# Performance work log

Hardware: AMD Instinct MI355X
Metric: run time of the kernel (lower is better)

Reference implementation:

```python
import jax, jax.numpy as jnp
import numpy as np

N_NODES = 100000
N_EDGES = 1600000
IN_DIM, HID_DIM, OUT_DIM = 128, 128, 64


def setup_inputs() -> dict:
    key = jax.random.key(0)
    k1, k2, k3, k4 = jax.random.split(key, 4)
    x = jax.random.normal(k1, (N_NODES, IN_DIM), dtype=jnp.float32)
    edge_index = jax.random.randint(k2, (2, N_EDGES), 0, N_NODES, dtype=jnp.int32)
    # Glorot-ish init for weights
    W1 = jax.random.normal(k3, (IN_DIM, HID_DIM), dtype=jnp.float32) / np.sqrt(IN_DIM)
    W2 = jax.random.normal(k4, (HID_DIM, OUT_DIM), dtype=jnp.float32) / np.sqrt(HID_DIM)
    b1 = jnp.zeros((HID_DIM,), dtype=jnp.float32)
    b2 = jnp.zeros((OUT_DIM,), dtype=jnp.float32)
    return {"x": x, "edge_index": edge_index, "W1": W1, "b1": b1, "W2": W2, "b2": b2}


def _gcn_norm(edge_index, num_nodes):
    # PyG gcn_norm: add self-loops, symmetric normalization deg^-1/2 A deg^-1/2
    loops = jnp.arange(num_nodes, dtype=edge_index.dtype)
    src = jnp.concatenate([edge_index[0], loops])  # [E+N]
    tgt = jnp.concatenate([edge_index[1], loops])
    deg = jax.ops.segment_sum(jnp.ones_like(tgt, dtype=jnp.float32), tgt,
                              num_segments=num_nodes)
    dinv = jnp.where(deg > 0, jax.lax.rsqrt(deg), 0.0)
    norm = dinv[src] * dinv[tgt]  # [E+N]
    return src, tgt, norm


def _gcn_conv(x, W, b, src, tgt, norm, num_nodes):
    h = x @ W                              # [N, D_out] transform first (GCNConv order)
    msg = norm[:, None] * h[src]           # gather + scale per edge
    agg = jax.ops.segment_sum(msg, tgt, num_segments=num_nodes)  # scatter-add
    return agg + b


def reference(x, edge_index, W1, b1, W2, b2):
    n = x.shape[0]
    src, tgt, norm = _gcn_norm(edge_index, n)
    h = jax.nn.relu(_gcn_conv(x, W1, b1, src, tgt, norm, n))
    out = _gcn_conv(h, W2, b2, src, tgt, norm, n)
    return out
```

## Files before the change

### kernel.cpp

```cpp
#include <hip/hip_runtime.h>


typedef unsigned int uint;
typedef unsigned short ushort;
typedef __attribute__((ext_vector_type(8))) short bf16x8;
typedef __attribute__((ext_vector_type(8))) ushort u16x8;
typedef __attribute__((ext_vector_type(4))) float f32x4;

#define BSHIFT 8
#define MAXBK  512
#define NB     256
#define CAP    8192

__device__ inline ushort f2bf(float f) {
    uint u = __float_as_uint(f);
    return (ushort)((u + 0x7fffu + ((u >> 16) & 1u)) >> 16);
}
__device__ inline float bf_lo(uint u) { return __uint_as_float(u << 16); }
__device__ inline float bf_hi(uint u) { return __uint_as_float(u & 0xffff0000u); }

__global__ __launch_bounds__(256) void hist_kernel(const int* __restrict__ tgt,
                                                   int* __restrict__ counts,
                                                   int E, int chunk, int nbk) {
    __shared__ int hist[MAXBK];
    int t = threadIdx.x, b = blockIdx.x;
    for (int i = t; i < nbk; i += 256) hist[i] = 0;
    __syncthreads();
    int s = b * chunk, e = min(E, s + chunk);
    int i = s + t * 4;
    for (; i + 3 < e; i += 1024) {
        int4 tv = *(const int4*)&tgt[i];
        atomicAdd(&hist[tv.x >> BSHIFT], 1);
        atomicAdd(&hist[tv.y >> BSHIFT], 1);
        atomicAdd(&hist[tv.z >> BSHIFT], 1);
        atomicAdd(&hist[tv.w >> BSHIFT], 1);
    }
    if (i < e)
        for (int k = i; k < e; ++k) atomicAdd(&hist[tgt[k] >> BSHIFT], 1);
    __syncthreads();
    for (int i2 = t; i2 < nbk; i2 += 256) counts[i2 * NB + b] = hist[i2];
}

__global__ __launch_bounds__(256) void scan_partial(const int* __restrict__ in,
                                                    int* __restrict__ bsum, int M) {
    int t = threadIdx.x, b = blockIdx.x;
    int base = b * 1024 + t * 4;
    int s = 0;
#pragma unroll
    for (int k = 0; k < 4; ++k) s += (base + k < M) ? in[base + k] : 0;
#pragma unroll
    for (int off = 32; off > 0; off >>= 1) s += __shfl_down(s, off, 64);
    __shared__ int ws[4];
    if ((t & 63) == 0) ws[t >> 6] = s;
    __syncthreads();
    if (t == 0) bsum[b] = ws[0] + ws[1] + ws[2] + ws[3];
}

__global__ __launch_bounds__(256) void scan_final_counts(int* __restrict__ counts,
                                                         const int* __restrict__ bsum,
                                                         int M) {
    int t = threadIdx.x, b = blockIdx.x;
    int lane = t & 63, wid = t >> 6;
    int p = 0;
    for (int i = t; i < b; i += 256) p += bsum[i];
#pragma unroll
    for (int off = 32; off > 0; off >>= 1) p += __shfl_down(p, off, 64);
    __shared__ int ps[4];
    if (lane == 0) ps[wid] = p;
    __syncthreads();
    int pre = ps[0] + ps[1] + ps[2] + ps[3];

    int base = b * 1024 + t * 4;
    int d[4];
#pragma unroll
    for (int k = 0; k < 4; ++k) d[k] = (base + k < M) ? counts[base + k] : 0;
    int tot = d[0] + d[1] + d[2] + d[3];
    int incl = tot;
#pragma unroll
    for (int off = 1; off < 64; off <<= 1) {
        int u = __shfl_up(incl, off, 64);
        if (lane >= off) incl += u;
    }
    __shared__ int wsum[4];
    if (lane == 63) wsum[wid] = incl;
    __syncthreads();
    int woff = 0;
    for (int w = 0; w < wid; ++w) woff += wsum[w];
    int run = incl - tot + woff + pre;
#pragma unroll
    for (int k = 0; k < 4; ++k) {
        if (base + k < M) counts[base + k] = run;
        run += d[k];
    }
}

__global__ __launch_bounds__(256) void bucket_scatter(const int* __restrict__ src,
                                                      const int* __restrict__ tgt,
                                                      const int* __restrict__ offsets,
                                                      int* __restrict__ tmpP,
                                                      int E, int chunk, int nbk) {
    __shared__ int cur[MAXBK];
    int t = threadIdx.x, b = blockIdx.x;
    for (int i = t; i < nbk; i += 256) cur[i] = offsets[i * NB + b];
    __syncthreads();
    int s = b * chunk, e = min(E, s + chunk);
    int i = s + t * 4;
    for (; i + 3 < e; i += 1024) {
        int4 sv = *(const int4*)&src[i];
        int4 tv = *(const int4*)&tgt[i];
        int p0 = atomicAdd(&cur[tv.x >> BSHIFT], 1);
        tmpP[p0] = (sv.x << BSHIFT) | (tv.x & 255);
        int p1 = atomicAdd(&cur[tv.y >> BSHIFT], 1);
        tmpP[p1] = (sv.y << BSHIFT) | (tv.y & 255);
        int p2 = atomicAdd(&cur[tv.z >> BSHIFT], 1);
        tmpP[p2] = (sv.z << BSHIFT) | (tv.z & 255);
        int p3 = atomicAdd(&cur[tv.w >> BSHIFT], 1);
        tmpP[p3] = (sv.w << BSHIFT) | (tv.w & 255);
    }
    if (i < e) {
        for (int k = i; k < e; ++k) {
            int tg = tgt[k];
            int p = atomicAdd(&cur[tg >> BSHIFT], 1);
            tmpP[p] = (src[k] << BSHIFT) | (tg & 255);
        }
    }
}

__global__ __launch_bounds__(256) void bucket_finish(const int* __restrict__ tmpP,
                                                     const int* __restrict__ offsets,
                                                     int* __restrict__ rowptr,
                                                     float* __restrict__ dinv,
                                                     int* __restrict__ csr_src,
                                                     int N, int E, int nbk) {
    __shared__ int stage[CAP];
    __shared__ int cnt[256];
    __shared__ int wsum[4];
    int t = threadIdx.x, b = blockIdx.x;
    cnt[t] = 0;
    __syncthreads();
    int s = offsets[b * NB];
    int e = (b + 1 < nbk) ? offsets[(b + 1) * NB] : E;
    int m = e - s;
    for (int i = t; i < m; i += 256) {
        int ed = tmpP[s + i];
        if (i < CAP) stage[i] = ed;
        atomicAdd(&cnt[ed & 255], 1);
    }
    __syncthreads();
    int lane = t & 63, wid = t >> 6;
    int d = cnt[t];
    int incl = d;
#pragma unroll
    for (int off = 1; off < 64; off <<= 1) {
        int u = __shfl_up(incl, off, 64);
        if (lane >= off) incl += u;
    }
    if (lane == 63) wsum[wid] = incl;
    __syncthreads();
    int woff = 0;
    for (int w = 0; w < wid; ++w) woff += wsum[w];
    int excl = s + incl - d + woff;
    int node = b * 256 + t;
    if (node < N) {
        rowptr[node] = excl;
        dinv[node] = rsqrtf((float)d + 1.0f);
    }
    if (b == nbk - 1 && t == 255) rowptr[N] = E;
    cnt[t] = excl;
    __syncthreads();
    for (int i = t; i < m; i += 256) {
        int ed = (i < CAP) ? stage[i] : tmpP[s + i];
        int p = atomicAdd(&cnt[ed & 255], 1);
        csr_src[p] = ed >> BSHIFT;
    }
}

template <int M, typename AT>
__global__ __launch_bounds__(256) void gemm_mfma(const AT* __restrict__ A,
                                                 const float* __restrict__ W,
                                                 const float* __restrict__ dinv,
                                                 ushort* __restrict__ C, int N) {
    constexpr int WTS = 136;
    __shared__ ushort WT[M * WTS];
    const int tid = threadIdx.x;
    for (int i = tid; i < 128 * (M / 4); i += 256) {
        int k = i / (M / 4);
        int n0 = (i % (M / 4)) * 4;
        float4 w = *(const float4*)&W[k * M + n0];
        WT[(n0 + 0) * WTS + k] = f2bf(w.x);
        WT[(n0 + 1) * WTS + k] = f2bf(w.y);
        WT[(n0 + 2) * WTS + k] = f2bf(w.z);
        WT[(n0 + 3) * WTS + k] = f2bf(w.w);
    }
    __syncthreads();

    const int wv = tid >> 6, lane = tid & 63;
    const int quad = lane >> 4, mrow = lane & 15;
    int arow_i = blockIdx.x * 64 + wv * 16 + mrow;
    if (arow_i >= N) arow_i = N - 1;

    f32x4 acc[M / 16];
#pragma unroll
    for (int t = 0; t < M / 16; ++t) acc[t] = (f32x4){0.f, 0.f, 0.f, 0.f};

#pragma unroll
    for (int ks = 0; ks < 4; ++ks) {
        const int k0 = ks * 32 + quad * 8;
        bf16x8 af;
        if constexpr (sizeof(AT) == 4) {
            const float* arow = (const float*)A + (size_t)arow_i * 128;
            float4 a0 = *(const float4*)&arow[k0];
            float4 a1 = *(const float4*)&arow[k0 + 4];
            af[0] = (short)f2bf(a0.x); af[1] = (short)f2bf(a0.y);
            af[2] = (short)f2bf(a0.z); af[3] = (short)f2bf(a0.w);
            af[4] = (short)f2bf(a1.x); af[5] = (short)f2bf(a1.y);
            af[6] = (short)f2bf(a1.z); af[7] = (short)f2bf(a1.w);
        } else {
            af = *(const bf16x8*)((const ushort*)A +
                                  ((size_t)(k0 >> 4) * N + arow_i) * 16 + (k0 & 15));
        }
#pragma unroll
        for (int t = 0; t < M / 16; ++t) {
            int n = t * 16 + mrow;
            bf16x8 bfr = *(const bf16x8*)&WT[n * WTS + k0];
            acc[t] = __builtin_amdgcn_mfma_f32_16x16x32_bf16(af, bfr, acc[t], 0, 0, 0);
        }
    }

    const int orow0 = blockIdx.x * 64 + wv * 16 + quad * 4;
#pragma unroll
    for (int r = 0; r < 4; ++r) {
        int orow = orow0 + r;
        if (orow < N) {
            float dv = dinv[orow];
#pragma unroll
            for (int t = 0; t < M / 16; ++t)
                C[((size_t)t * N + orow) * 16 + mrow] = f2bf(dv * acc[t][r]);
        }
    }
}

template <int D, bool RELU, bool OUTBF>
__global__ __launch_bounds__(128) void gather_sliced(
    const ushort* __restrict__ h, const int* __restrict__ rowptr,
    const int* __restrict__ csr_src, const float* __restrict__ dinv,
    const float* __restrict__ bias, void* __restrict__ outv, int N) {
    constexpr int NS = D / 16;
    constexpr int CAPE = 2048;
    __shared__ int eL[CAPE];
    const int tid = threadIdx.x;
    const int base = blockIdx.x * 64;
    const int bbeg = rowptr[base];
    const int bend = rowptr[min(base + 64, N)];
    const int m = bend - bbeg;
    for (int i = tid; i < m && i < CAPE; i += 128) eL[i] = csr_src[bbeg + i];
    __syncthreads();

    const int node = base + (tid >> 1);
    const int q = tid & 1;
    const int qoff = q * 8;
    const bool alive = node < N;
    int beg = 0, end = 0;
    float di = 0.f;
    if (alive) {
        beg = rowptr[node];
        end = rowptr[node + 1];
        di = dinv[node];
    }

    auto acc8 = [](float* a, uint4 v) {
        a[0] += bf_lo(v.x); a[1] += bf_hi(v.x);
        a[2] += bf_lo(v.y); a[3] += bf_hi(v.y);
        a[4] += bf_lo(v.z); a[5] += bf_hi(v.z);
        a[6] += bf_lo(v.w); a[7] += bf_hi(v.w);
    };

    auto run = [&](auto LD) {
#pragma unroll 1
        for (int s = 0; s < NS; ++s) {
            const ushort* hs = h + (size_t)s * N * 16;
            float acc[8] = {};
            if (alive) {
                int j = beg;
                for (; j + 1 < end; j += 2) {
                    int s0 = LD(j), s1 = LD(j + 1);
                    uint4 va = *(const uint4*)&hs[(size_t)s0 * 16 + qoff];
                    uint4 vb = *(const uint4*)&hs[(size_t)s1 * 16 + qoff];
                    acc8(acc, va);
                    acc8(acc, vb);
                }
                if (j < end) {
                    int s0 = LD(j);
                    acc8(acc, *(const uint4*)&hs[(size_t)s0 * 16 + qoff]);
                }
                acc8(acc, *(const uint4*)&hs[(size_t)node * 16 + qoff]);

                float4 b0 = *(const float4*)&bias[s * 16 + qoff];
                float4 b1 = *(const float4*)&bias[s * 16 + qoff + 4];
                float r[8] = {di * acc[0] + b0.x, di * acc[1] + b0.y,
                              di * acc[2] + b0.z, di * acc[3] + b0.w,
                              di * acc[4] + b1.x, di * acc[5] + b1.y,
                              di * acc[6] + b1.z, di * acc[7] + b1.w};
                if (RELU) {
#pragma unroll
                    for (int k = 0; k < 8; ++k) r[k] = fmaxf(r[k], 0.0f);
                }
                if constexpr (OUTBF) {
                    ushort* out = (ushort*)outv;
                    u16x8 o;
#pragma unroll
                    for (int k = 0; k < 8; ++k) o[k] = f2bf(r[k]);
                    *(u16x8*)&out[((size_t)s * N + node) * 16 + qoff] = o;
                } else {
                    float* out = (float*)outv;
                    *(float4*)&out[(size_t)node * D + s * 16 + qoff] =
                        make_float4(r[0], r[1], r[2], r[3]);
                    *(float4*)&out[(size_t)node * D + s * 16 + qoff + 4] =
                        make_float4(r[4], r[5], r[6], r[7]);
                }
            }
        }
    };

    if (m <= CAPE)
        run([&](int j) { return eL[j - bbeg]; });
    else
        run([&](int j) { return csr_src[j]; });
}

extern "C" void kernel_launch(void* const* d_in, const int* in_sizes, int n_in,
                              void* d_out, int out_size, void* d_ws, size_t ws_size,
                              hipStream_t stream) {
    const float* x  = (const float*)d_in[0];
    const int*   ei = (const int*)d_in[1];
    const float* W1 = (const float*)d_in[2];
    const float* b1 = (const float*)d_in[3];
    const float* W2 = (const float*)d_in[4];
    const float* b2 = (const float*)d_in[5];
    float* out = (float*)d_out;

    const int N = in_sizes[0] / 128;
    const int E = in_sizes[1] / 2;
    const int* src = ei;
    const int* tgt = ei + E;

    const int nbk   = (N + 255) >> BSHIFT;
    const int chunk = (((E + NB - 1) / NB) + 3) & ~3;
    const int Mc    = nbk * NB;

    float* ws = (float*)d_ws;
    const size_t Np = (size_t)((N + 3) & ~3);
    float*  dinv    = ws;
    int*    rowptr  = (int*)(ws + Np);
    int*    counts  = rowptr + Np + 4;
    int*    bsum    = counts + MAXBK * NB;
    int*    csr_src = bsum + 128;
    int*    tmpP    = csr_src + E;
    ushort* h       = (ushort*)(tmpP + E);
    ushort* h1      = h + (size_t)N * 128;
    ushort* h2      = h;

    const int nbc = (Mc + 1023) / 1024;

    hist_kernel<<<NB, 256, 0, stream>>>(tgt, counts, E, chunk, nbk);
    scan_partial<<<nbc, 256, 0, stream>>>(counts, bsum, Mc);
    scan_final_counts<<<nbc, 256, 0, stream>>>(counts, bsum, Mc);
    bucket_scatter<<<NB, 256, 0, stream>>>(src, tgt, counts, tmpP, E, chunk, nbk);
    bucket_finish<<<nbk, 256, 0, stream>>>(tmpP, counts, rowptr, dinv, csr_src, N, E, nbk);

    const int ngb = (N + 63) / 64;

    gemm_mfma<128, float><<<(N + 63) / 64, 256, 0, stream>>>(x, W1, dinv, h, N);
    gather_sliced<128, true, true><<<ngb, 128, 0, stream>>>(
        h, rowptr, csr_src, dinv, b1, h1, N);

    gemm_mfma<64, ushort><<<(N + 63) / 64, 256, 0, stream>>>(h1, W2, dinv, h2, N);
    gather_sliced<64, false, false><<<ngb, 128, 0, stream>>>(
        h2, rowptr, csr_src, dinv, b2, out, N);
}
```

Measured before the change: 343.3 us.

## Split gather feature slices across blocks and widen node tiles

The aggregation kernel now assigns each feature slice to its own block instead of looping over slices inside one block. Each block covers 128 nodes with 256 threads, a larger edge-index staging buffer and a 4-way unrolled neighbour loop. This gives many more concurrent waves to hide the latency of the irregular gathers. In exchange every block reloads the same edge list, and the 64-wide second layer launches 8 slice blocks although it has only 4 slices, so half of those blocks repeat work and write identical results.

```diff
diff --git a/kernel.cpp b/kernel.cpp
--- a/kernel.cpp
+++ b/kernel.cpp
@@ -241,91 +241,85 @@
 }
 
 template <int D, bool RELU, bool OUTBF>
-__global__ __launch_bounds__(128) void gather_sliced(
+__global__ __launch_bounds__(256) void gather_part(
     const ushort* __restrict__ h, const int* __restrict__ rowptr,
     const int* __restrict__ csr_src, const float* __restrict__ dinv,
     const float* __restrict__ bias, void* __restrict__ outv, int N) {
     constexpr int NS = D / 16;
-    constexpr int CAPE = 2048;
+    constexpr int CAPE = 4096;
     __shared__ int eL[CAPE];
     const int tid = threadIdx.x;
-    const int base = blockIdx.x * 64;
+    const int sl = blockIdx.x & 7;
+    const int s  = sl & (NS - 1);
+    const int nb = blockIdx.x >> 3;
+    const int base = nb * 128;
     const int bbeg = rowptr[base];
-    const int bend = rowptr[min(base + 64, N)];
+    const int bend = rowptr[min(base + 128, N)];
     const int m = bend - bbeg;
-    for (int i = tid; i < m && i < CAPE; i += 128) eL[i] = csr_src[bbeg + i];
+    for (int i = tid; i < m && i < CAPE; i += 256) eL[i] = csr_src[bbeg + i];
     __syncthreads();
 
     const int node = base + (tid >> 1);
+    if (node >= N) return;
     const int q = tid & 1;
     const int qoff = q * 8;
-    const bool alive = node < N;
-    int beg = 0, end = 0;
-    float di = 0.f;
-    if (alive) {
-        beg = rowptr[node];
-        end = rowptr[node + 1];
-        di = dinv[node];
-    }
-
-    auto acc8 = [](float* a, uint4 v) {
-        a[0] += bf_lo(v.x); a[1] += bf_hi(v.x);
-        a[2] += bf_lo(v.y); a[3] += bf_hi(v.y);
-        a[4] += bf_lo(v.z); a[5] += bf_hi(v.z);
-        a[6] += bf_lo(v.w); a[7] += bf_hi(v.w);
+    const int beg = rowptr[node], end = rowptr[node + 1];
+    const float di = dinv[node];
+    const ushort* hs = h + (size_t)s * N * 16;
+
+    float acc[8] = {};
+    auto acc8 = [&](uint4 v) {
+        acc[0] += bf_lo(v.x); acc[1] += bf_hi(v.x);
+        acc[2] += bf_lo(v.y); acc[3] += bf_hi(v.y);
+        acc[4] += bf_lo(v.z); acc[5] += bf_hi(v.z);
+        acc[6] += bf_lo(v.w); acc[7] += bf_hi(v.w);
     };
 
-    auto run = [&](auto LD) {
-#pragma unroll 1
-        for (int s = 0; s < NS; ++s) {
-            const ushort* hs = h + (size_t)s * N * 16;
-            float acc[8] = {};
-            if (alive) {
-                int j = beg;
-                for (; j + 1 < end; j += 2) {
-                    int s0 = LD(j), s1 = LD(j + 1);
-                    uint4 va = *(const uint4*)&hs[(size_t)s0 * 16 + qoff];
-                    uint4 vb = *(const uint4*)&hs[(size_t)s1 * 16 + qoff];
-                    acc8(acc, va);
-                    acc8(acc, vb);
-                }
-                if (j < end) {
-                    int s0 = LD(j);
-                    acc8(acc, *(const uint4*)&hs[(size_t)s0 * 16 + qoff]);
-                }
-                acc8(acc, *(const uint4*)&hs[(size_t)node * 16 + qoff]);
-
-                float4 b0 = *(const float4*)&bias[s * 16 + qoff];
-                float4 b1 = *(const float4*)&bias[s * 16 + qoff + 4];
-                float r[8] = {di * acc[0] + b0.x, di * acc[1] + b0.y,
-                              di * acc[2] + b0.z, di * acc[3] + b0.w,
-                              di * acc[4] + b1.x, di * acc[5] + b1.y,
-                              di * acc[6] + b1.z, di * acc[7] + b1.w};
-                if (RELU) {
-#pragma unroll
-                    for (int k = 0; k < 8; ++k) r[k] = fmaxf(r[k], 0.0f);
-                }
-                if constexpr (OUTBF) {
-                    ushort* out = (ushort*)outv;
-                    u16x8 o;
-#pragma unroll
-                    for (int k = 0; k < 8; ++k) o[k] = f2bf(r[k]);
-                    *(u16x8*)&out[((size_t)s * N + node) * 16 + qoff] = o;
-                } else {
-                    float* out = (float*)outv;
-                    *(float4*)&out[(size_t)node * D + s * 16 + qoff] =
-                        make_float4(r[0], r[1], r[2], r[3]);
-                    *(float4*)&out[(size_t)node * D + s * 16 + qoff + 4] =
-                        make_float4(r[4], r[5], r[6], r[7]);
-                }
-            }
+    auto body = [&](auto LD) {
+        int j = beg;
+        for (; j + 3 < end; j += 4) {
+            int s0 = LD(j), s1 = LD(j + 1), s2 = LD(j + 2), s3 = LD(j + 3);
+            uint4 v0 = *(const uint4*)&hs[(size_t)s0 * 16 + qoff];
+            uint4 v1 = *(const uint4*)&hs[(size_t)s1 * 16 + qoff];
+            uint4 v2 = *(const uint4*)&hs[(size_t)s2 * 16 + qoff];
+            uint4 v3 = *(const uint4*)&hs[(size_t)s3 * 16 + qoff];
+            acc8(v0); acc8(v1); acc8(v2); acc8(v3);
+        }
+        for (; j < end; ++j) {
+            int s0 = LD(j);
+            acc8(*(const uint4*)&hs[(size_t)s0 * 16 + qoff]);
         }
     };
-
     if (m <= CAPE)
-        run([&](int j) { return eL[j - bbeg]; });
+        body([&](int j) { return eL[j - bbeg]; });
     else
-        run([&](int j) { return csr_src[j]; });
+        body([&](int j) { return csr_src[j]; });
+
+    acc8(*(const uint4*)&hs[(size_t)node * 16 + qoff]);
+
+    float4 b0 = *(const float4*)&bias[s * 16 + qoff];
+    float4 b1 = *(const float4*)&bias[s * 16 + qoff + 4];
+    float r[8] = {di * acc[0] + b0.x, di * acc[1] + b0.y,
+                  di * acc[2] + b0.z, di * acc[3] + b0.w,
+                  di * acc[4] + b1.x, di * acc[5] + b1.y,
+                  di * acc[6] + b1.z, di * acc[7] + b1.w};
+    if (RELU) {
+#pragma unroll
+        for (int k = 0; k < 8; ++k) r[k] = fmaxf(r[k], 0.0f);
+    }
+    if constexpr (OUTBF) {
+        ushort* out = (ushort*)outv;
+        u16x8 o;
+#pragma unroll
+        for (int k = 0; k < 8; ++k) o[k] = f2bf(r[k]);
+        *(u16x8*)&out[((size_t)s * N + node) * 16 + qoff] = o;
+    } else {
+        float* out = (float*)outv;
+        *(float4*)&out[(size_t)node * D + s * 16 + qoff] =
+            make_float4(r[0], r[1], r[2], r[3]);
+        *(float4*)&out[(size_t)node * D + s * 16 + qoff + 4] =
+            make_float4(r[4], r[5], r[6], r[7]);
+    }
 }
 
 extern "C" void kernel_launch(void* const* d_in, const int* in_sizes, int n_in,
@@ -368,13 +362,13 @@
     bucket_scatter<<<NB, 256, 0, stream>>>(src, tgt, counts, tmpP, E, chunk, nbk);
     bucket_finish<<<nbk, 256, 0, stream>>>(tmpP, counts, rowptr, dinv, csr_src, N, E, nbk);
 
-    const int ngb = (N + 63) / 64;
+    const int ngb = (N + 127) / 128;
 
     gemm_mfma<128, float><<<(N + 63) / 64, 256, 0, stream>>>(x, W1, dinv, h, N);
-    gather_sliced<128, true, true><<<ngb, 128, 0, stream>>>(
+    gather_part<128, true, true><<<ngb * 8, 256, 0, stream>>>(
         h, rowptr, csr_src, dinv, b1, h1, N);
 
     gemm_mfma<64, ushort><<<(N + 63) / 64, 256, 0, stream>>>(h1, W2, dinv, h2, N);
-    gather_sliced<64, false, false><<<ngb, 128, 0, stream>>>(
+    gather_part<64, false, false><<<ngb * 8, 256, 0, stream>>>(
         h2, rowptr, csr_src, dinv, b2, out, N);
 }
```

After: 339.5 us. No clear change (-1.1%).
